# Performance work log

Hardware: AMD Instinct MI355X
Metric: run time of the kernel (lower is better)

## Reference

```python
import jax, jax.numpy as jnp
import numpy as np

N_NODES = 100000
N_EDGES = 800000
EPS = 1e-5


def _mean_agg(h, src, dst):
    # DGL SAGEConv 'mean': average of in-neighbor features per dst node.
    msg = jnp.take(h, src, axis=0)                      # [E, D] gather
    summed = jax.ops.segment_sum(msg, dst, num_segments=N_NODES)
    deg = jax.ops.segment_sum(jnp.ones((src.shape[0],), h.dtype), dst,
                              num_segments=N_NODES)
    return summed / jnp.maximum(deg, 1.0)[:, None]


def _sage(h, src, dst, ws, wn, b):
    # rst = fc_self(h) + fc_neigh(mean_neigh) + bias
    return h @ ws + _mean_agg(h, src, dst) @ wn + b


def _bn(x, g, b, m, v):
    return (x - m) * (g / jnp.sqrt(v + EPS)) + b


def setup_inputs() -> dict:
    key = jax.random.key(0)
    ks = jax.random.split(key, 16)
    s = 0.02
    inp = {
        "structural_features": jax.random.normal(ks[0], (N_NODES, 128), jnp.float32),
        "multimodal_features": jax.random.normal(ks[1], (N_NODES, 384), jnp.float32),
        "src": jax.random.randint(ks[2], (N_EDGES,), 0, N_NODES),
        "dst": jax.random.randint(ks[3], (N_EDGES,), 0, N_NODES),
        "enc_w": jax.random.normal(ks[4], (512, 128), jnp.float32) * s,
        "enc_b": jnp.zeros((128,), jnp.float32),
        "sage0_ws": jax.random.normal(ks[5], (128, 256), jnp.float32) * s,
        "sage0_wn": jax.random.normal(ks[6], (128, 256), jnp.float32) * s,
        "sage0_b": jnp.zeros((256,), jnp.float32),
        "bn0_g": jnp.ones((256,), jnp.float32),
        "bn0_b": jnp.zeros((256,), jnp.float32),
        "bn0_m": jnp.zeros((256,), jnp.float32),
        "bn0_v": jnp.ones((256,), jnp.float32),
        "sage1_ws": jax.random.normal(ks[7], (256, 128), jnp.float32) * s,
        "sage1_wn": jax.random.normal(ks[8], (256, 128), jnp.float32) * s,
        "sage1_b": jnp.zeros((128,), jnp.float32),
        "bn1_g": jnp.ones((128,), jnp.float32),
        "bn1_b": jnp.zeros((128,), jnp.float32),
        "bn1_m": jnp.zeros((128,), jnp.float32),
        "bn1_v": jnp.ones((128,), jnp.float32),
        "rel_w": jax.random.normal(ks[9], (256, 128), jnp.float32) * s,
        "rel_b": jnp.zeros((128,), jnp.float32),
        "cls_w1": jax.random.normal(ks[10], (128, 64), jnp.float32) * s,
        "cls_b1": jnp.zeros((64,), jnp.float32),
        "cls_w2": jax.random.normal(ks[11], (64, 32), jnp.float32) * s,
        "cls_b2": jnp.zeros((32,), jnp.float32),
    }
    return inp


def reference(structural_features, multimodal_features, src, dst,
              enc_w, enc_b,
              sage0_ws, sage0_wn, sage0_b, bn0_g, bn0_b, bn0_m, bn0_v,
              sage1_ws, sage1_wn, sage1_b, bn1_g, bn1_b, bn1_m, bn1_v,
              rel_w, rel_b, cls_w1, cls_b1, cls_w2, cls_b2):
    x = jnp.concatenate([structural_features, multimodal_features], axis=-1)
    h0 = jax.nn.relu(x @ enc_w + enc_b)                     # input_encoder (dropout=eval)
    h = jax.nn.relu(_bn(_sage(h0, src, dst, sage0_ws, sage0_wn, sage0_b),
                        bn0_g, bn0_b, bn0_m, bn0_v))
    h = jax.nn.relu(_bn(_sage(h, src, dst, sage1_ws, sage1_wn, sage1_b),
                        bn1_g, bn1_b, bn1_m, bn1_v))
    h_final = jnp.concatenate([h0, h], axis=1)              # [N, 256]
    h_final = jax.nn.relu(h_final @ rel_w + rel_b)          # relation_encoder
    out = jax.nn.relu(h_final @ cls_w1 + cls_b1) @ cls_w2 + cls_b2
    return out
```

## Files before the change

kernel.cpp:

```cpp
#include <hip/hip_runtime.h>
#include <math.h>


#define EPS 1e-5f

typedef __attribute__((ext_vector_type(8))) short bf16x8;
typedef __attribute__((ext_vector_type(4))) float f32x4;

__device__ inline unsigned short f2bf(float x) {
    unsigned u = __float_as_uint(x);
    u += 0x7fff + ((u >> 16) & 1);
    return (unsigned short)(u >> 16);
}
__device__ inline float bf2f(unsigned short h) {
    return __uint_as_float(((unsigned)h) << 16);
}
__device__ inline unsigned packbf(float x, float y) {
    return (unsigned)f2bf(x) | ((unsigned)f2bf(y) << 16);
}

__device__ inline void gload_lds16(const void* g, void* l) {
    __builtin_amdgcn_global_load_lds(
        (__attribute__((address_space(1))) void*)g,
        (__attribute__((address_space(3))) void*)l, 16, 0, 0);
}


__global__ void count_deg(const int* __restrict__ dst, int* __restrict__ deg, int e) {
    int i = blockIdx.x * 256 + threadIdx.x;
    if (i < e) atomicAdd(&deg[dst[i]], 1);
}

__global__ __launch_bounds__(1024)
void scan_block(const int* __restrict__ deg, int* __restrict__ rowptr,
                int* __restrict__ part, int n) {
    __shared__ int buf[1024];
    const int tid = threadIdx.x;
    const int i = blockIdx.x * 1024 + tid;
    const int v = (i < n) ? deg[i] : 0;
    buf[tid] = v;
    __syncthreads();
    #pragma unroll 1
    for (int off = 1; off < 1024; off <<= 1) {
        int t = (tid >= off) ? buf[tid - off] : 0;
        __syncthreads();
        buf[tid] += t;
        __syncthreads();
    }
    if (i < n) rowptr[i] = buf[tid] - v;
    if (tid == 1023) part[blockIdx.x] = buf[1023];
}

__global__ __launch_bounds__(1024)
void scan_part(int* __restrict__ part, int nb) {
    __shared__ int buf[1024];
    const int tid = threadIdx.x;
    const int v = (tid < nb) ? part[tid] : 0;
    buf[tid] = v;
    __syncthreads();
    #pragma unroll 1
    for (int off = 1; off < 1024; off <<= 1) {
        int t = (tid >= off) ? buf[tid - off] : 0;
        __syncthreads();
        buf[tid] += t;
        __syncthreads();
    }
    if (tid < nb) part[tid] = buf[tid] - v;
    if (tid == 1023) part[nb] = buf[1023];
}

__global__ void scan_add(const int* __restrict__ part, int* __restrict__ rowptr,
                         int* __restrict__ cursor, int n, int nb) {
    int i = blockIdx.x * 256 + threadIdx.x;
    if (i < n) {
        int v = rowptr[i] + part[i >> 10];
        rowptr[i] = v;
        cursor[i] = v;
    }
    if (i == 0) rowptr[n] = part[nb];
}

__global__ void fill_edges(const int* __restrict__ src, const int* __restrict__ dst,
                           int* __restrict__ cursor, int* __restrict__ eidx, int e) {
    int i = blockIdx.x * 256 + threadIdx.x;
    if (i < e) {
        int pos = atomicAdd(&cursor[dst[i]], 1);
        eidx[pos] = src[i];
    }
}


__global__ __launch_bounds__(256)
void prep_all(const float* __restrict__ enc_w, const float* __restrict__ s0_ws,
              const float* __restrict__ s0_wn, const float* __restrict__ s1_ws,
              const float* __restrict__ s1_wn, const float* __restrict__ rel_w,
              const float* __restrict__ cw1, const float* __restrict__ cw2,
              short* wt_enc_h, short* wt_enc_l, short* wt_s0_h, short* wt_s0_l,
              short* wt_st_h, short* wt_st_l, short* wt_rel_h, short* wt_rel_l,
              short* wt_c1_h, short* wt_c1_l, short* wt_c2_h, short* wt_c2_l) {
    int e = blockIdx.x * 256 + threadIdx.x;
    const float* W; short* hi; short* lo; int Nd, ldt, koff;
    if (e < 65536)       { W = enc_w; hi = wt_enc_h; lo = wt_enc_l; Nd = 128; ldt = 512; koff = 0; }
    else if (e < 98304)  { e -= 65536;  W = s0_ws; hi = wt_s0_h; lo = wt_s0_l; Nd = 256; ldt = 256; koff = 0; }
    else if (e < 131072) { e -= 98304;  W = s0_wn; hi = wt_s0_h; lo = wt_s0_l; Nd = 256; ldt = 256; koff = 128; }
    else if (e < 163840) { e -= 131072; W = s1_ws; hi = wt_st_h; lo = wt_st_l; Nd = 128; ldt = 256; koff = 0; }
    else if (e < 196608) { e -= 163840; W = s1_wn; hi = wt_st_h + 32768; lo = wt_st_l + 32768; Nd = 128; ldt = 256; koff = 0; }
    else if (e < 229376) { e -= 196608; W = rel_w; hi = wt_rel_h; lo = wt_rel_l; Nd = 128; ldt = 256; koff = 0; }
    else if (e < 237568) { e -= 229376; W = cw1; hi = wt_c1_h; lo = wt_c1_l; Nd = 64; ldt = 128; koff = 0; }
    else if (e < 239616) { e -= 237568; W = cw2; hi = wt_c2_h; lo = wt_c2_l; Nd = 32; ldt = 64; koff = 0; }
    else return;
    const int k = e / Nd, n = e - k * Nd;
    const float x = W[e];
    const unsigned short h = f2bf(x);
    const unsigned short l = f2bf(x - bf2f(h));
    const size_t o = (size_t)n * ldt + koff + k;
    hi[o] = (short)h;
    lo[o] = (short)l;
}


__global__ __launch_bounds__(256)
void concat_bf16(const float* __restrict__ sf, const float* __restrict__ mf,
                 short* __restrict__ xb, int nn) {
    const int S = nn * 16;
    const int g = blockIdx.x * 256 + threadIdx.x;
    if (g >= S) return;
    const int q = g & 63;
    float4 f[4][2];
    #pragma unroll
    for (int j = 0; j < 4; ++j) {
        const int n = (g + j * S) >> 6;
        const float* p = (q < 16) ? (sf + (size_t)n * 128 + (size_t)q * 8)
                                  : (mf + (size_t)n * 384 + (size_t)(q - 16) * 8);
        f[j][0] = ((const float4*)p)[0];
        f[j][1] = ((const float4*)p)[1];
    }
    #pragma unroll
    for (int j = 0; j < 4; ++j) {
        uint4 o;
        o.x = packbf(f[j][0].x, f[j][0].y); o.y = packbf(f[j][0].z, f[j][0].w);
        o.z = packbf(f[j][1].x, f[j][1].y); o.w = packbf(f[j][1].z, f[j][1].w);
        *(uint4*)(xb + (size_t)(g + j * S) * 8) = o;
    }
}


__global__ __launch_bounds__(256)
void agg_mean_bb(const short* __restrict__ featb,
                 const int* __restrict__ rowptr, const int* __restrict__ eidx,
                 short* __restrict__ outb, int n) {
    const int node = blockIdx.x * 4 + (threadIdx.x >> 6);
    if (node >= n) return;
    const int lane = threadIdx.x & 63;
    const int g = lane >> 4, j = lane & 15;
    const int beg = rowptr[node], end = rowptr[node + 1];
    float s[8];
    #pragma unroll
    for (int i = 0; i < 8; ++i) s[i] = 0.f;
    for (int e = beg + g; e < end; e += 4) {
        const uint4 v = *(const uint4*)(featb + (size_t)eidx[e] * 128 + j * 8);
        s[0] += __uint_as_float(v.x << 16); s[1] += __uint_as_float(v.x & 0xffff0000u);
        s[2] += __uint_as_float(v.y << 16); s[3] += __uint_as_float(v.y & 0xffff0000u);
        s[4] += __uint_as_float(v.z << 16); s[5] += __uint_as_float(v.z & 0xffff0000u);
        s[6] += __uint_as_float(v.w << 16); s[7] += __uint_as_float(v.w & 0xffff0000u);
    }
    #pragma unroll
    for (int i = 0; i < 8; ++i) {
        s[i] += __shfl_xor(s[i], 32);
        s[i] += __shfl_xor(s[i], 16);
    }
    if (g == 0) {
        const float inv = 1.0f / fmaxf((float)(end - beg), 1.0f);
        uint4 o;
        o.x = packbf(s[0] * inv, s[1] * inv);
        o.y = packbf(s[2] * inv, s[3] * inv);
        o.z = packbf(s[4] * inv, s[5] * inv);
        o.w = packbf(s[6] * inv, s[7] * inv);
        *(uint4*)(outb + (size_t)node * 128 + j * 8) = o;
    }
}

__global__ __launch_bounds__(256)
void agg_combine_bb(const short* __restrict__ featb,
                    const int* __restrict__ rowptr, const int* __restrict__ eidx,
                    const float* __restrict__ s1,
                    const float* __restrict__ bias,
                    const float* __restrict__ bng, const float* __restrict__ bnb,
                    const float* __restrict__ bnm, const float* __restrict__ bnv,
                    short* __restrict__ outb, int n) {
    const int node = blockIdx.x * 4 + (threadIdx.x >> 6);
    if (node >= n) return;
    const int lane = threadIdx.x & 63;
    const int g = lane >> 4, j = lane & 15;
    const int beg = rowptr[node], end = rowptr[node + 1];
    float s[8];
    #pragma unroll
    for (int i = 0; i < 8; ++i) s[i] = 0.f;
    for (int e = beg + g; e < end; e += 4) {
        const uint4 v = *(const uint4*)(featb + (size_t)eidx[e] * 128 + j * 8);
        s[0] += __uint_as_float(v.x << 16); s[1] += __uint_as_float(v.x & 0xffff0000u);
        s[2] += __uint_as_float(v.y << 16); s[3] += __uint_as_float(v.y & 0xffff0000u);
        s[4] += __uint_as_float(v.z << 16); s[5] += __uint_as_float(v.z & 0xffff0000u);
        s[6] += __uint_as_float(v.w << 16); s[7] += __uint_as_float(v.w & 0xffff0000u);
    }
    #pragma unroll
    for (int i = 0; i < 8; ++i) {
        s[i] += __shfl_xor(s[i], 32);
        s[i] += __shfl_xor(s[i], 16);
    }
    if (g == 0) {
        const float inv = 1.0f / fmaxf((float)(end - beg), 1.0f);
        const int c0 = j * 8;
        const float4 a0 = *(const float4*)(s1 + (size_t)node * 128 + c0);
        const float4 a1 = *(const float4*)(s1 + (size_t)node * 128 + c0 + 4);
        const float sf[8] = {a0.x, a0.y, a0.z, a0.w, a1.x, a1.y, a1.z, a1.w};
        float r[8];
        #pragma unroll
        for (int i = 0; i < 8; ++i) {
            const int c = c0 + i;
            float v = sf[i] + s[i] * inv + bias[c];
            v = (v - bnm[c]) * (bng[c] / sqrtf(bnv[c] + EPS)) + bnb[c];
            r[i] = fmaxf(v, 0.f);
        }
        uint4 o;
        o.x = packbf(r[0], r[1]); o.y = packbf(r[2], r[3]);
        o.z = packbf(r[4], r[5]); o.w = packbf(r[6], r[7]);
        *(uint4*)(outb + (size_t)node * 128 + j * 8) = o;
    }
}

template<int NT, int K1, int K2>
__global__ __launch_bounds__(256)
void gemm_dp(const short* __restrict__ A1, int lda1,
             const short* __restrict__ A2, int lda2,
             const short* __restrict__ Wt_hi, const short* __restrict__ Wt_lo,
             const float* __restrict__ bias,
             const float* __restrict__ bng, const float* __restrict__ bnb,
             const float* __restrict__ bnm, const float* __restrict__ bnv,
             int relu,
             float* __restrict__ Cf, int fpN, int ldc,
             short* __restrict__ Cb, int bfcol0, int ldcb,
             int M) {
    constexpr int K   = K1 + K2;
    constexpr int NBK = K / 64;
    constexpr int NTW = NT / 2;
    static_assert(K % 64 == 0, "K multiple of 64");
    static_assert(NT % 2 == 0, "NT even");
    static_assert(K2 == 0 || K1 % 64 == 0, "concat boundary on BK");
    constexpr int ASZ = 128 * 64;
    constexpr int BSZ = 2 * NT * 16 * 64;
    constexpr int BUF = ASZ + BSZ;
    __shared__ short lds[2 * BUF];

    const int tid  = threadIdx.x;
    const int lane = tid & 63;
    const int wv   = tid >> 6;
    const int wm   = wv >> 1;
    const int wn   = wv & 1;
    const int bm   = blockIdx.y * 128;
    const int col0 = blockIdx.x * (NT * 16);
    const int lrow = lane & 15;
    const int quad = lane >> 4;

    const int su = (tid & 7) ^ ((tid >> 3) & 7);
    const short* gsA1[4];
    const short* gsA2[4];
    #pragma unroll
    for (int jj = 0; jj < 4; ++jj) {
        const int rg = min(bm + jj * 32 + (tid >> 3), M - 1);
        gsA1[jj] = A1 + (size_t)rg * lda1 + su * 8;
        if constexpr (K2 > 0) gsA2[jj] = A2 + (size_t)rg * lda2 + su * 8;
        else gsA2[jj] = nullptr;
    }
    const short* gsB[NT];
    #pragma unroll
    for (int jj = 0; jj < NT; ++jj) {
        const int colIdx = jj * 32 + (tid >> 3);
        const bool ishi = colIdx < NT * 16;
        const int cp = ishi ? colIdx : colIdx - NT * 16;
        gsB[jj] = (ishi ? Wt_hi : Wt_lo) + (size_t)(col0 + cp) * K + su * 8;
    }

    auto stage = [&](int b, int c) {
        const int k = c * 64;
        #pragma unroll
        for (int jj = 0; jj < 4; ++jj) {
            const short* p;
            if constexpr (K2 > 0)
                p = (k < K1) ? (gsA1[jj] + k) : (gsA2[jj] + (k - K1));
            else
                p = gsA1[jj] + k;
            gload_lds16(p, &lds[b * BUF + (jj * 256 + tid) * 8]);
        }
        #pragma unroll
        for (int jj = 0; jj < NT; ++jj)
            gload_lds16(gsB[jj] + k, &lds[b * BUF + ASZ + (jj * 256 + tid) * 8]);
    };

    int aoff[4][2];
    #pragma unroll
    for (int m = 0; m < 4; ++m)
        #pragma unroll
        for (int kk = 0; kk < 2; ++kk)
            aoff[m][kk] = (wm * 64 + m * 16 + lrow) * 64 +
                          (((kk * 4 + quad) ^ (lrow & 7)) * 8);
    int boff[NTW][2];
    #pragma unroll
    for (int nt = 0; nt < NTW; ++nt)
        #pragma unroll
        for (int kk = 0; kk < 2; ++kk)
            boff[nt][kk] = (wn * NTW * 16 + nt * 16 + lrow) * 64 +
                           (((kk * 4 + quad) ^ (lrow & 7)) * 8);

    f32x4 acc[4][NTW];
    #pragma unroll
    for (int m = 0; m < 4; ++m)
        #pragma unroll
        for (int nt = 0; nt < NTW; ++nt)
            acc[m][nt] = (f32x4){0.f, 0.f, 0.f, 0.f};

    stage(0, 0);

    for (int c = 0; c < NBK; ++c) {
        const int b = c & 1;
        if (c + 1 < NBK) {
            stage(b ^ 1, c + 1);
            if constexpr (NT == 4) asm volatile("s_waitcnt vmcnt(8)" ::: "memory");
            else                   asm volatile("s_waitcnt vmcnt(6)" ::: "memory");
        } else {
            asm volatile("s_waitcnt vmcnt(0)" ::: "memory");
        }
        __builtin_amdgcn_s_barrier();

        const short* La = &lds[b * BUF];
        const short* Lb = &lds[b * BUF + ASZ];
        #pragma unroll
        for (int kk = 0; kk < 2; ++kk) {
            bf16x8 a[4];
            #pragma unroll
            for (int m = 0; m < 4; ++m)
                a[m] = *(const bf16x8*)(La + aoff[m][kk]);
            #pragma unroll
            for (int nt = 0; nt < NTW; ++nt) {
                const bf16x8 vbh = *(const bf16x8*)(Lb + boff[nt][kk]);
                const bf16x8 vbl = *(const bf16x8*)(Lb + boff[nt][kk] + NT * 16 * 64);
                #pragma unroll
                for (int m = 0; m < 4; ++m) {
                    acc[m][nt] = __builtin_amdgcn_mfma_f32_16x16x32_bf16(a[m], vbh, acc[m][nt], 0, 0, 0);
                    acc[m][nt] = __builtin_amdgcn_mfma_f32_16x16x32_bf16(a[m], vbl, acc[m][nt], 0, 0, 0);
                }
            }
        }
        asm volatile("" ::: "memory");
        __builtin_amdgcn_s_barrier();
    }

    constexpr int EW = NT * 16 + 4;
    float* ep = (float*)lds;

    #pragma unroll
    for (int nt = 0; nt < NTW; ++nt) {
        const int lcol = wn * NTW * 16 + nt * 16 + lrow;
        const int gcol = col0 + lcol;
        const float bsc = bias ? bias[gcol] : 0.f;
        float gg = 1.f, bb = 0.f, mm = 0.f;
        if (bng) { gg = bng[gcol] / sqrtf(bnv[gcol] + EPS); bb = bnb[gcol]; mm = bnm[gcol]; }
        #pragma unroll
        for (int m = 0; m < 4; ++m) {
            #pragma unroll
            for (int r = 0; r < 4; ++r) {
                float x = acc[m][nt][r] + bsc;
                if (bng) x = (x - mm) * gg + bb;
                if (relu) x = fmaxf(x, 0.f);
                ep[(wm * 64 + m * 16 + quad * 4 + r) * EW + lcol] = x;
            }
        }
    }
    __syncthreads();

    if (col0 < fpN) {
        for (int g = tid; g < 128 * NT * 4; g += 256) {
            const int row = g / (NT * 4), u = g - row * (NT * 4);
            const int grow = bm + row;
            if (grow < M)
                *(float4*)(Cf + (size_t)grow * ldc + col0 + u * 4) =
                    *(const float4*)(ep + row * EW + u * 4);
        }
    } else {
        for (int g = tid; g < 128 * NT * 2; g += 256) {
            const int row = g / (NT * 2), u = g - row * (NT * 2);
            const int grow = bm + row;
            const float4 f0 = *(const float4*)(ep + row * EW + u * 8);
            const float4 f1 = *(const float4*)(ep + row * EW + u * 8 + 4);
            uint4 o;
            o.x = packbf(f0.x, f0.y); o.y = packbf(f0.z, f0.w);
            o.z = packbf(f1.x, f1.y); o.w = packbf(f1.z, f1.w);
            if (grow < M)
                *(uint4*)(Cb + (size_t)grow * ldcb + (col0 - bfcol0) + u * 8) = o;
        }
    }
}


extern "C" void kernel_launch(void* const* d_in, const int* in_sizes, int n_in,
                              void* d_out, int out_size, void* d_ws, size_t ws_size,
                              hipStream_t stream) {
    const float* sf    = (const float*)d_in[0];
    const float* mf    = (const float*)d_in[1];
    const int*   src   = (const int*)d_in[2];
    const int*   dst   = (const int*)d_in[3];
    const float* enc_w = (const float*)d_in[4];
    const float* enc_b = (const float*)d_in[5];
    const float* s0_ws = (const float*)d_in[6];
    const float* s0_wn = (const float*)d_in[7];
    const float* s0_b  = (const float*)d_in[8];
    const float* bn0_g = (const float*)d_in[9];
    const float* bn0_b = (const float*)d_in[10];
    const float* bn0_m = (const float*)d_in[11];
    const float* bn0_v = (const float*)d_in[12];
    const float* s1_ws = (const float*)d_in[13];
    const float* s1_wn = (const float*)d_in[14];
    const float* s1_b  = (const float*)d_in[15];
    const float* bn1_g = (const float*)d_in[16];
    const float* bn1_b = (const float*)d_in[17];
    const float* bn1_m = (const float*)d_in[18];
    const float* bn1_v = (const float*)d_in[19];
    const float* rel_w = (const float*)d_in[20];
    const float* rel_b = (const float*)d_in[21];
    const float* cw1   = (const float*)d_in[22];
    const float* cb1   = (const float*)d_in[23];
    const float* cw2   = (const float*)d_in[24];
    const float* cb2   = (const float*)d_in[25];
    float* out = (float*)d_out;

    const int nn = in_sizes[0] / 128;
    const int ne = in_sizes[2];
    const int nb = (nn + 1023) / 1024;

    short* h0b   = (short*)d_ws;
    short* xb    = h0b + (size_t)nn * 128;
    float* st    = (float*)xb;
    short* h1b   = (short*)(st + (size_t)nn * 128);
    short* agg0b = xb + (size_t)nn * 512;
    short* t1b   = agg0b + (size_t)nn * 128;
    short* h2b   = t1b + (size_t)nn * 128;
    short* o1b   = agg0b;
    short* rb    = t1b;
    int* deg    = (int*)(h2b + (size_t)nn * 128);
    int* rowptr = deg + nn;
    int* cursor = rowptr + nn + 1;
    int* part   = cursor + nn;
    int* eidx   = part + nb + 1;
    short* wts = (short*)(eidx + ne);
    short* wt_enc_h = wts;                 short* wt_enc_l = wt_enc_h + 65536;
    short* wt_s0_h  = wt_enc_l + 65536;    short* wt_s0_l  = wt_s0_h  + 65536;
    short* wt_st_h  = wt_s0_l  + 65536;    short* wt_st_l  = wt_st_h  + 65536;
    short* wt_rel_h = wt_st_l  + 65536;    short* wt_rel_l = wt_rel_h + 32768;
    short* wt_c1_h  = wt_rel_l + 32768;    short* wt_c1_l  = wt_c1_h  + 8192;
    short* wt_c2_h  = wt_c1_l  + 8192;     short* wt_c2_l  = wt_c2_h  + 2048;

    const dim3 blk(256);
    const int gM = (nn + 127) / 128;

    hipMemsetAsync(deg, 0, (size_t)nn * 4, stream);
    count_deg <<<dim3((ne + 255) / 256), blk, 0, stream>>>(dst, deg, ne);
    scan_block<<<dim3(nb), dim3(1024), 0, stream>>>(deg, rowptr, part, nn);
    scan_part <<<dim3(1),  dim3(1024), 0, stream>>>(part, nb);
    scan_add  <<<dim3((nn + 255) / 256), blk, 0, stream>>>(part, rowptr, cursor, nn, nb);
    fill_edges<<<dim3((ne + 255) / 256), blk, 0, stream>>>(src, dst, cursor, eidx, ne);

    prep_all<<<dim3(936), blk, 0, stream>>>(
        enc_w, s0_ws, s0_wn, s1_ws, s1_wn, rel_w, cw1, cw2,
        wt_enc_h, wt_enc_l, wt_s0_h, wt_s0_l, wt_st_h, wt_st_l,
        wt_rel_h, wt_rel_l, wt_c1_h, wt_c1_l, wt_c2_h, wt_c2_l);

    concat_bf16<<<dim3((nn * 16 + 255) / 256), blk, 0, stream>>>(sf, mf, xb, nn);

    gemm_dp<4, 512, 0><<<dim3(2, gM), blk, 0, stream>>>(
        xb, 512, nullptr, 0, wt_enc_h, wt_enc_l, enc_b,
        nullptr, nullptr, nullptr, nullptr, 1,
        nullptr, 0, 0, h0b, 0, 128, nn);

    agg_mean_bb<<<dim3((nn + 3) / 4), blk, 0, stream>>>(
        h0b, rowptr, eidx, agg0b, nn);

    gemm_dp<4, 128, 128><<<dim3(4, gM), blk, 0, stream>>>(
        h0b, 128, agg0b, 128, wt_s0_h, wt_s0_l, s0_b,
        bn0_g, bn0_b, bn0_m, bn0_v, 1,
        nullptr, 0, 0, h1b, 0, 256, nn);

    gemm_dp<4, 256, 0><<<dim3(4, gM), blk, 0, stream>>>(
        h1b, 256, nullptr, 0, wt_st_h, wt_st_l, nullptr,
        nullptr, nullptr, nullptr, nullptr, 0,
        st, 128, 128, t1b, 128, 128, nn);

    agg_combine_bb<<<dim3((nn + 3) / 4), blk, 0, stream>>>(
        t1b, rowptr, eidx, st, s1_b,
        bn1_g, bn1_b, bn1_m, bn1_v, h2b, nn);

    gemm_dp<4, 128, 128><<<dim3(2, gM), blk, 0, stream>>>(
        h0b, 128, h2b, 128, wt_rel_h, wt_rel_l, rel_b,
        nullptr, nullptr, nullptr, nullptr, 1,
        nullptr, 0, 0, rb, 0, 128, nn);

    gemm_dp<4, 128, 0><<<dim3(1, gM), blk, 0, stream>>>(
        rb, 128, nullptr, 0, wt_c1_h, wt_c1_l, cb1,
        nullptr, nullptr, nullptr, nullptr, 1,
        nullptr, 0, 0, o1b, 0, 64, nn);

    gemm_dp<2, 64, 0><<<dim3(1, gM), blk, 0, stream>>>(
        o1b, 64, nullptr, 0, wt_c2_h, wt_c2_l, cb2,
        nullptr, nullptr, nullptr, nullptr, 0,
        out, 32, 32, nullptr, 0, 0, nn);
}
```

Before: 699.2 us.

## Fuse classifier MLP GEMMs and pipeline concat conversion through LDS

Replaces the two classifier GEMM launches with one gemm_cls kernel. It keeps the 64-wide ReLU hidden layer in LDS and runs the second matmul directly from it, so the intermediate bf16 buffer is never written to or read back from global memory, and one launch is removed. It also rewrites concat_bf16 as a persistent grid-stride kernel that double-buffers the fp32 inputs into LDS with async global-to-LDS loads before converting them to bf16. The risks are that the new concat assumes nn is a multiple of 4, and the second layer's B operands are read straight from global memory without staging.

```diff
diff --git a/kernel.cpp b/kernel.cpp
--- a/kernel.cpp
+++ b/kernel.cpp
@@ -122,25 +122,49 @@
 __global__ __launch_bounds__(256)
 void concat_bf16(const float* __restrict__ sf, const float* __restrict__ mf,
                  short* __restrict__ xb, int nn) {
-    const int S = nn * 16;
-    const int g = blockIdx.x * 256 + threadIdx.x;
-    if (g >= S) return;
-    const int q = g & 63;
-    float4 f[4][2];
-    #pragma unroll
-    for (int j = 0; j < 4; ++j) {
-        const int n = (g + j * S) >> 6;
-        const float* p = (q < 16) ? (sf + (size_t)n * 128 + (size_t)q * 8)
-                                  : (mf + (size_t)n * 384 + (size_t)(q - 16) * 8);
-        f[j][0] = ((const float4*)p)[0];
-        f[j][1] = ((const float4*)p)[1];
-    }
-    #pragma unroll
-    for (int j = 0; j < 4; ++j) {
+    __shared__ float lds[2 * 2048];
+    const int t = threadIdx.x;
+    const int nIter = nn >> 2;
+
+    const float* P1; size_t ld1;
+    if (t < 128) { P1 = sf + (size_t)(t >> 5) * 128 + (t & 31) * 4; ld1 = 128; }
+    else { const int em = t - 128;
+           P1 = mf + (size_t)(em / 96) * 384 + (em % 96) * 4; ld1 = 384; }
+    const int em2 = t + 128;
+    const float* P2 = mf + (size_t)(em2 / 96) * 384 + (em2 % 96) * 4;
+
+    const int n = t >> 6, q = t & 63;
+    const int raddr = (q < 16) ? (n * 128 + q * 8)
+                               : (512 + n * 384 + (q - 16) * 8);
+
+    int it = blockIdx.x;
+    if (it >= nIter) return;
+    {
+        const size_t r0 = (size_t)it * 4;
+        gload_lds16(P1 + r0 * ld1, (char*)lds + t * 16);
+        gload_lds16(P2 + r0 * 384, (char*)lds + 4096 + t * 16);
+    }
+    int b = 0;
+    for (; it < nIter; it += gridDim.x) {
+        const int nx = it + gridDim.x;
+        if (nx < nIter) {
+            const size_t r0 = (size_t)nx * 4;
+            gload_lds16(P1 + r0 * ld1, (char*)lds + (b ^ 1) * 8192 + t * 16);
+            gload_lds16(P2 + r0 * 384, (char*)lds + (b ^ 1) * 8192 + 4096 + t * 16);
+            asm volatile("s_waitcnt vmcnt(2)" ::: "memory");
+        } else {
+            asm volatile("s_waitcnt vmcnt(0)" ::: "memory");
+        }
+        __builtin_amdgcn_s_barrier();
+        const float* base = lds + b * 2048 + raddr;
+        const float4 f0 = *(const float4*)base;
+        const float4 f1 = *(const float4*)(base + 4);
         uint4 o;
-        o.x = packbf(f[j][0].x, f[j][0].y); o.y = packbf(f[j][0].z, f[j][0].w);
-        o.z = packbf(f[j][1].x, f[j][1].y); o.w = packbf(f[j][1].z, f[j][1].w);
-        *(uint4*)(xb + (size_t)(g + j * S) * 8) = o;
+        o.x = packbf(f0.x, f0.y); o.y = packbf(f0.z, f0.w);
+        o.z = packbf(f1.x, f1.y); o.w = packbf(f1.z, f1.w);
+        *(uint4*)(xb + ((size_t)it * 256 + t) * 8) = o;
+        __builtin_amdgcn_s_barrier();
+        b ^= 1;
     }
 }
 
@@ -398,6 +422,168 @@
             if (grow < M)
                 *(uint4*)(Cb + (size_t)grow * ldcb + (col0 - bfcol0) + u * 8) = o;
         }
+    }
+}
+
+__global__ __launch_bounds__(256)
+void gemm_cls(const short* __restrict__ A1,
+              const short* __restrict__ W1h, const short* __restrict__ W1l,
+              const float* __restrict__ cb1,
+              const short* __restrict__ W2h, const short* __restrict__ W2l,
+              const float* __restrict__ cb2,
+              float* __restrict__ out, int M) {
+    constexpr int NT = 4, NTW = 2, NBK = 2, K = 128;
+    constexpr int ASZ = 128 * 64, BSZ = 2 * NT * 16 * 64, BUF = ASZ + BSZ;
+    __shared__ short lds[2 * BUF];
+
+    const int tid  = threadIdx.x;
+    const int lane = tid & 63;
+    const int wv   = tid >> 6;
+    const int wm   = wv >> 1;
+    const int wn   = wv & 1;
+    const int bm   = blockIdx.x * 128;
+    const int lrow = lane & 15;
+    const int quad = lane >> 4;
+
+    const int su = (tid & 7) ^ ((tid >> 3) & 7);
+    const short* gsA[4];
+    #pragma unroll
+    for (int jj = 0; jj < 4; ++jj) {
+        const int rg = min(bm + jj * 32 + (tid >> 3), M - 1);
+        gsA[jj] = A1 + (size_t)rg * 128 + su * 8;
+    }
+    const short* gsB[NT];
+    #pragma unroll
+    for (int jj = 0; jj < NT; ++jj) {
+        const int colIdx = jj * 32 + (tid >> 3);
+        const bool ishi = colIdx < NT * 16;
+        const int cp = ishi ? colIdx : colIdx - NT * 16;
+        gsB[jj] = (ishi ? W1h : W1l) + (size_t)cp * K + su * 8;
+    }
+    auto stage = [&](int b, int c) {
+        const int k = c * 64;
+        #pragma unroll
+        for (int jj = 0; jj < 4; ++jj)
+            gload_lds16(gsA[jj] + k, &lds[b * BUF + (jj * 256 + tid) * 8]);
+        #pragma unroll
+        for (int jj = 0; jj < NT; ++jj)
+            gload_lds16(gsB[jj] + k, &lds[b * BUF + ASZ + (jj * 256 + tid) * 8]);
+    };
+
+    int aoff[4][2], boff[NTW][2];
+    #pragma unroll
+    for (int m = 0; m < 4; ++m)
+        #pragma unroll
+        for (int kk = 0; kk < 2; ++kk)
+            aoff[m][kk] = (wm * 64 + m * 16 + lrow) * 64 +
+                          (((kk * 4 + quad) ^ (lrow & 7)) * 8);
+    #pragma unroll
+    for (int nt = 0; nt < NTW; ++nt)
+        #pragma unroll
+        for (int kk = 0; kk < 2; ++kk)
+            boff[nt][kk] = (wn * NTW * 16 + nt * 16 + lrow) * 64 +
+                           (((kk * 4 + quad) ^ (lrow & 7)) * 8);
+
+    f32x4 acc[4][NTW];
+    #pragma unroll
+    for (int m = 0; m < 4; ++m)
+        #pragma unroll
+        for (int nt = 0; nt < NTW; ++nt)
+            acc[m][nt] = (f32x4){0.f, 0.f, 0.f, 0.f};
+
+    stage(0, 0);
+    for (int c = 0; c < NBK; ++c) {
+        const int b = c & 1;
+        if (c + 1 < NBK) {
+            stage(b ^ 1, c + 1);
+            asm volatile("s_waitcnt vmcnt(8)" ::: "memory");
+        } else {
+            asm volatile("s_waitcnt vmcnt(0)" ::: "memory");
+        }
+        __builtin_amdgcn_s_barrier();
+        const short* La = &lds[b * BUF];
+        const short* Lb = &lds[b * BUF + ASZ];
+        #pragma unroll
+        for (int kk = 0; kk < 2; ++kk) {
+            bf16x8 a[4];
+            #pragma unroll
+            for (int m = 0; m < 4; ++m)
+                a[m] = *(const bf16x8*)(La + aoff[m][kk]);
+            #pragma unroll
+            for (int nt = 0; nt < NTW; ++nt) {
+                const bf16x8 vbh = *(const bf16x8*)(Lb + boff[nt][kk]);
+                const bf16x8 vbl = *(const bf16x8*)(Lb + boff[nt][kk] + NT * 16 * 64);
+                #pragma unroll
+                for (int m = 0; m < 4; ++m) {
+                    acc[m][nt] = __builtin_amdgcn_mfma_f32_16x16x32_bf16(a[m], vbh, acc[m][nt], 0, 0, 0);
+                    acc[m][nt] = __builtin_amdgcn_mfma_f32_16x16x32_bf16(a[m], vbl, acc[m][nt], 0, 0, 0);
+                }
+            }
+        }
+        asm volatile("" ::: "memory");
+        __builtin_amdgcn_s_barrier();
+    }
+
+    constexpr int EW = 68;
+    float* ep = (float*)lds;
+    #pragma unroll
+    for (int nt = 0; nt < NTW; ++nt) {
+        const int lcol = wn * NTW * 16 + nt * 16 + lrow;
+        const float bsc = cb1[lcol];
+        #pragma unroll
+        for (int m = 0; m < 4; ++m)
+            #pragma unroll
+            for (int r = 0; r < 4; ++r)
+                ep[(wm * 64 + m * 16 + quad * 4 + r) * EW + lcol] =
+                    fmaxf(acc[m][nt][r] + bsc, 0.f);
+    }
+    __syncthreads();
+
+    const short* pB2h = W2h + (size_t)(wn * 16 + lrow) * 64 + quad * 8;
+    const short* pB2l = W2l + (size_t)(wn * 16 + lrow) * 64 + quad * 8;
+    f32x4 acc2[4];
+    #pragma unroll
+    for (int m = 0; m < 4; ++m) acc2[m] = (f32x4){0.f, 0.f, 0.f, 0.f};
+    #pragma unroll
+    for (int kk = 0; kk < 2; ++kk) {
+        const bf16x8 bh = *(const bf16x8*)(pB2h + kk * 32);
+        const bf16x8 bl = *(const bf16x8*)(pB2l + kk * 32);
+        #pragma unroll
+        for (int m = 0; m < 4; ++m) {
+            const float* pe = ep + (wm * 64 + m * 16 + lrow) * EW + kk * 32 + quad * 8;
+            const float4 e0 = *(const float4*)pe;
+            const float4 e1 = *(const float4*)(pe + 4);
+            bf16x8 a;
+            a[0] = (short)f2bf(e0.x); a[1] = (short)f2bf(e0.y);
+            a[2] = (short)f2bf(e0.z); a[3] = (short)f2bf(e0.w);
+            a[4] = (short)f2bf(e1.x); a[5] = (short)f2bf(e1.y);
+            a[6] = (short)f2bf(e1.z); a[7] = (short)f2bf(e1.w);
+            acc2[m] = __builtin_amdgcn_mfma_f32_16x16x32_bf16(a, bh, acc2[m], 0, 0, 0);
+            acc2[m] = __builtin_amdgcn_mfma_f32_16x16x32_bf16(a, bl, acc2[m], 0, 0, 0);
+        }
+    }
+
+    constexpr int EW2 = 36;
+    float* ep2 = (float*)lds + 128 * EW;
+    {
+        const int lcol = wn * 16 + lrow;
+        const float bsc = cb2[lcol];
+        #pragma unroll
+        for (int m = 0; m < 4; ++m)
+            #pragma unroll
+            for (int r = 0; r < 4; ++r)
+                ep2[(wm * 64 + m * 16 + quad * 4 + r) * EW2 + lcol] =
+                    acc2[m][r] + bsc;
+    }
+    __syncthreads();
+    #pragma unroll
+    for (int j = 0; j < 4; ++j) {
+        const int g = tid + j * 256;
+        const int row = g >> 3, u = g & 7;
+        const int grow = bm + row;
+        if (grow < M)
+            *(float4*)(out + (size_t)grow * 32 + u * 4) =
+                *(const float4*)(ep2 + row * EW2 + u * 4);
     }
 }
 
@@ -444,7 +630,6 @@
     short* agg0b = xb + (size_t)nn * 512;
     short* t1b   = agg0b + (size_t)nn * 128;
     short* h2b   = t1b + (size_t)nn * 128;
-    short* o1b   = agg0b;
     short* rb    = t1b;
     int* deg    = (int*)(h2b + (size_t)nn * 128);
     int* rowptr = deg + nn;
@@ -474,7 +659,7 @@
         wt_enc_h, wt_enc_l, wt_s0_h, wt_s0_l, wt_st_h, wt_st_l,
         wt_rel_h, wt_rel_l, wt_c1_h, wt_c1_l, wt_c2_h, wt_c2_l);
 
-    concat_bf16<<<dim3((nn * 16 + 255) / 256), blk, 0, stream>>>(sf, mf, xb, nn);
+    concat_bf16<<<dim3(2048), blk, 0, stream>>>(sf, mf, xb, nn);
 
     gemm_dp<4, 512, 0><<<dim3(2, gM), blk, 0, stream>>>(
         xb, 512, nullptr, 0, wt_enc_h, wt_enc_l, enc_b,
@@ -503,13 +688,6 @@
         nullptr, nullptr, nullptr, nullptr, 1,
         nullptr, 0, 0, rb, 0, 128, nn);
 
-    gemm_dp<4, 128, 0><<<dim3(1, gM), blk, 0, stream>>>(
-        rb, 128, nullptr, 0, wt_c1_h, wt_c1_l, cb1,
-        nullptr, nullptr, nullptr, nullptr, 1,
-        nullptr, 0, 0, o1b, 0, 64, nn);
-
-    gemm_dp<2, 64, 0><<<dim3(1, gM), blk, 0, stream>>>(
-        o1b, 64, nullptr, 0, wt_c2_h, wt_c2_l, cb2,
-        nullptr, nullptr, nullptr, nullptr, 0,
-        out, 32, 32, nullptr, 0, 0, nn);
-}
+    gemm_cls<<<dim3(gM), blk, 0, stream>>>(
+        rb, wt_c1_h, wt_c1_l, cb1, wt_c2_h, wt_c2_l, cb2, out, nn);
+}
```

After: 691.8 us. No clear change (-1.1%).
